# Performance work log

Measured on AMD Instinct MI355X. Metric: run time of the kernel, lower is better.

The kernel has to match this reference:

```python
import jax, jax.numpy as jnp
import numpy as np

N, E, IN_DIM, OUT_DIM, R = 50000, 800000, 128, 128, 8


def setup_inputs() -> dict:
    key = jax.random.key(0)
    k1, k2, k3, k4, k5 = jax.random.split(key, 5)
    x = jax.random.normal(k1, (N, IN_DIM), dtype=jnp.float32)
    edge_index = jax.random.randint(k2, (2, E), 0, N, dtype=jnp.int32)
    edge_type = jax.random.randint(k3, (E,), 0, R, dtype=jnp.int32)
    # Xavier-uniform-ish init for parameters
    lim_w = float(np.sqrt(6.0 / (IN_DIM + OUT_DIM)))
    weight = jax.random.uniform(k4, (R, IN_DIM, OUT_DIM), dtype=jnp.float32, minval=-lim_w, maxval=lim_w)
    self_weight = jax.random.uniform(k5, (IN_DIM, OUT_DIM), dtype=jnp.float32, minval=-lim_w, maxval=lim_w)
    return {"x": x, "weight": weight, "self_weight": self_weight,
            "edge_index": edge_index, "edge_type": edge_type}


def reference(x, weight, self_weight, edge_index, edge_type):
    n = x.shape[0]
    r = weight.shape[0]
    d_out = weight.shape[2]
    src, dst = edge_index[0], edge_index[1]
    # undirected: symmetrize edges (directed=False)
    src_all = jnp.concatenate([src, dst])          # [2E]
    dst_all = jnp.concatenate([dst, src])          # [2E]
    et_all = jnp.concatenate([edge_type, edge_type])  # [2E]
    # transform all nodes by every relation weight once: [R, N, D_out]
    xw = jnp.einsum('ni,rio->rno', x, weight)
    # gather per-edge messages already transformed by their relation's W_r
    msg = xw[et_all, src_all]                      # [2E, D_out]
    # fused (relation, dst) segment id -> per-relation scatter-add
    seg = et_all.astype(jnp.int32) * n + dst_all
    agg = jax.ops.segment_sum(msg, seg, num_segments=r * n).reshape(r, n, d_out)
    deg = jax.ops.segment_sum(jnp.ones_like(seg, dtype=x.dtype), seg,
                              num_segments=r * n).reshape(r, n)
    deg_inv = jnp.where(deg > 0, 1.0 / jnp.maximum(deg, 1.0), jnp.zeros_like(deg))
    out = jnp.sum(agg * deg_inv[..., None], axis=0)  # [N, D_out]
    out = out + x @ self_weight                       # self-loop
    return out
```

## Files before the change

### kernel.cpp

```cpp
#include <hip/hip_runtime.h>

#define NN 50000
#define EE 800000
#define RR 8
#define DD 128
#define SS (NN*RR)
#define TE (2*EE)
#define NB 782
#define NBLK 391
#define NS (NB*NBLK)

typedef __attribute__((ext_vector_type(8))) short bf16x8;
typedef __attribute__((ext_vector_type(4))) float f32x4;

__device__ __forceinline__ unsigned short f2bf(float f){
  unsigned int u = __float_as_uint(f);
  u += 0x7fffu + ((u >> 16) & 1u);
  return (unsigned short)(u >> 16);
}
__device__ __forceinline__ float bf_lo(unsigned int w){ return __uint_as_float(w << 16); }
__device__ __forceinline__ float bf_hi(unsigned int w){ return __uint_as_float(w & 0xffff0000u); }

__device__ __forceinline__ void acc8(float* a, uint4 u){
  a[0] += bf_lo(u.x); a[1] += bf_hi(u.x);
  a[2] += bf_lo(u.y); a[3] += bf_hi(u.y);
  a[4] += bf_lo(u.z); a[5] += bf_hi(u.z);
  a[6] += bf_lo(u.w); a[7] += bf_hi(u.w);
}
__device__ __forceinline__ unsigned int pack2(float a, float b){
  return ((unsigned int)f2bf(b) << 16) | (unsigned int)f2bf(a);
}

__device__ __forceinline__ void dir_edge(const int* ei, const int* et, int j,
                                         int& s, int& d, int& t){
  if (j < EE){ s = ei[j]; d = ei[EE + j]; t = et[j]; }
  else { int jj = j - EE; s = ei[EE + jj]; d = ei[jj]; t = et[jj]; }
}

__global__ __launch_bounds__(256) void k_hist(const int* __restrict__ ei,
                                              const int* __restrict__ et,
                                              int* __restrict__ hist){
  __shared__ int h[NB];
  int tid = threadIdx.x, bid = blockIdx.x;
  for (int i = tid; i < NB; i += 256) h[i] = 0;
  __syncthreads();
  int j0 = bid*4096;
  for (int k = tid; k < 4096; k += 256){
    int j = j0 + k;
    if (j < TE){
      int s, d, t; dir_edge(ei, et, j, s, d, t);
      atomicAdd(&h[d >> 6], 1);
    }
  }
  __syncthreads();
  for (int i = tid; i < NB; i += 256) hist[i*NBLK + bid] = h[i];
}

__global__ __launch_bounds__(256) void k_scan1(int* __restrict__ hist,
                                               int* __restrict__ blksum){
  __shared__ int sd[256];
  int b = blockIdx.x, tid = threadIdx.x;
  int base = b*1024 + tid*4;
  int v0 = (base+0 < NS) ? hist[base+0] : 0;
  int v1 = (base+1 < NS) ? hist[base+1] : 0;
  int v2 = (base+2 < NS) ? hist[base+2] : 0;
  int v3 = (base+3 < NS) ? hist[base+3] : 0;
  int ts = v0+v1+v2+v3;
  sd[tid] = ts; __syncthreads();
  for (int o = 1; o < 256; o <<= 1){
    int t = (tid >= o) ? sd[tid-o] : 0;
    __syncthreads();
    sd[tid] += t;
    __syncthreads();
  }
  int ex = sd[tid] - ts;
  if (base+0 < NS) hist[base+0] = ex; ex += v0;
  if (base+1 < NS) hist[base+1] = ex; ex += v1;
  if (base+2 < NS) hist[base+2] = ex; ex += v2;
  if (base+3 < NS) hist[base+3] = ex;
  if (tid == 255) blksum[b] = sd[255];
}

__global__ __launch_bounds__(512) void k_scan2(int* __restrict__ blksum, int nb){
  __shared__ int sd[512];
  int tid = threadIdx.x;
  int v = (tid < nb) ? blksum[tid] : 0;
  sd[tid] = v; __syncthreads();
  for (int o = 1; o < 512; o <<= 1){
    int t = (tid >= o) ? sd[tid-o] : 0;
    __syncthreads();
    sd[tid] += t;
    __syncthreads();
  }
  if (tid < nb) blksum[tid] = sd[tid] - v;
}

__global__ __launch_bounds__(256) void k_scan3(int* __restrict__ hist,
                                               const int* __restrict__ blksum){
  int i = blockIdx.x*blockDim.x + threadIdx.x;
  if (i < NS) hist[i] += blksum[i >> 10];
}

__global__ __launch_bounds__(256) void k_part(const int* __restrict__ ei,
                                              const int* __restrict__ et,
                                              const int* __restrict__ S,
                                              unsigned int* __restrict__ P){
  __shared__ int cur[NB];
  int tid = threadIdx.x, bid = blockIdx.x;
  for (int i = tid; i < NB; i += 256) cur[i] = S[i*NBLK + bid];
  __syncthreads();
  int j0 = bid*4096;
  for (int k = tid; k < 4096; k += 256){
    int j = j0 + k;
    if (j < TE){
      int s, d, t; dir_edge(ei, et, j, s, d, t);
      int b = d >> 6;
      int p = atomicAdd(&cur[b], 1);
      P[p] = (unsigned int)s | ((unsigned int)(d & 63) << 17)
           | ((unsigned int)t << 23);
    }
  }
}

__global__ __launch_bounds__(256) void k_build(const unsigned int* __restrict__ P,
                                               const int* __restrict__ S,
                                               int* __restrict__ esrc,
                                               int* __restrict__ offs){
  __shared__ int h[512], cu[512], sd[256];
  int tid = threadIdx.x, b = blockIdx.x;
  int pstart = S[b*NBLK];
  int pend   = (b+1 < NB) ? S[(b+1)*NBLK] : TE;
  int ne = pend - pstart;
  h[2*tid] = 0; h[2*tid+1] = 0;
  __syncthreads();
  for (int k = tid; k < ne; k += 256){
    unsigned int u = P[pstart + k];
    int lseg = (int)(((u >> 17) & 63u)*8u + (u >> 23));
    atomicAdd(&h[lseg], 1);
  }
  __syncthreads();
  int v0 = h[2*tid], v1 = h[2*tid+1];
  int ts = v0 + v1;
  sd[tid] = ts; __syncthreads();
  for (int o = 1; o < 256; o <<= 1){
    int t = (tid >= o) ? sd[tid-o] : 0;
    __syncthreads();
    sd[tid] += t;
    __syncthreads();
  }
  int ex = sd[tid] - ts;
  cu[2*tid]   = pstart + ex;
  cu[2*tid+1] = pstart + ex + v0;
  int seg0 = b*512;
  if (seg0 + 2*tid     < SS) offs[seg0 + 2*tid]     = cu[2*tid];
  if (seg0 + 2*tid + 1 < SS) offs[seg0 + 2*tid + 1] = cu[2*tid+1];
  if (b == NB-1 && tid == 0) offs[SS] = TE;
  __syncthreads();
  for (int k = tid; k < ne; k += 256){
    unsigned int u = P[pstart + k];
    int lseg = (int)(((u >> 17) & 63u)*8u + (u >> 23));
    int r = atomicAdd(&cu[lseg], 1);
    esrc[r] = (int)(u & 0x1ffffu);
  }
}

__global__ __launch_bounds__(256) void k_conv(const float* __restrict__ x,
                                              const float* __restrict__ w,
                                              const float* __restrict__ sw,
                                              unsigned short* __restrict__ xb,
                                              unsigned short* __restrict__ wb){
  int i = blockIdx.x*blockDim.x + threadIdx.x;
  const int M1 = NN*DD/4;
  if (i < M1){
    float4 v = ((const float4*)x)[i];
    ushort4 o;
    o.x = f2bf(v.x); o.y = f2bf(v.y); o.z = f2bf(v.z); o.w = f2bf(v.w);
    ((ushort4*)xb)[i] = o;
  } else {
    int j = i - M1;
    if (j < 9*DD*DD){
      int r = j >> 14; int rem = j & 16383; int n = rem >> 7; int k = rem & 127;
      float v = (r < 8) ? w[r*16384 + k*128 + n] : sw[k*128 + n];
      wb[j] = f2bf(v);
    }
  }
}

__global__ __launch_bounds__(256, 3) void k_fused(
    const unsigned short* __restrict__ xb,
    const unsigned short* __restrict__ wb,
    const int* __restrict__ offs,
    const int* __restrict__ esrc,
    float* __restrict__ out)
{
  __shared__ __align__(16) unsigned short Alds[2][32][136];
  const int tid  = threadIdx.x;
  const int wave = tid >> 6, lane = tid & 63;
  const int l15  = lane & 15, quad = lane >> 4;
  const int g    = quad;
  const int gl   = l15;
  const int lb   = g << 4;
  const int rowbase = blockIdx.x * 32;

  uint4 selfU[2];
  #pragma unroll
  for (int p = 0; p < 2; ++p){
    int gd = rowbase + wave*8 + 2*g + p;
    selfU[p] = make_uint4(0u,0u,0u,0u);
    if (gd < NN) selfU[p] = *(const uint4*)(xb + (size_t)gd*DD + gl*8);
  }

  int sidx = (rowbase + wave*8)*8 + lane;
  int voff = 0, vcnt = 0;
  if (sidx < SS){
    voff = offs[sidx];
    vcnt = offs[sidx + 1] - voff;
  }

  int idxbuf[2][2];
  uint4 U[2][8];

  auto issue_idx = [&](int rq, int bi){
    #pragma unroll
    for (int p = 0; p < 2; ++p){
      int sl  = (2*g + p)*8 + rq;
      int off = __shfl(voff, sl);
      int cnt = __shfl(vcnt, sl);
      idxbuf[bi][p] = 0;
      if (gl < cnt) idxbuf[bi][p] = esrc[off + gl];
    }
  };

  auto issue_bursts = [&](int rq, int bi){
    #pragma unroll
    for (int p = 0; p < 2; ++p){
      int sl  = (2*g + p)*8 + rq;
      int cnt = __shfl(vcnt, sl);
      int cm  = cnt < 8 ? cnt : 8;
      #pragma unroll
      for (int e = 0; e < 8; ++e){
        U[p][e] = make_uint4(0u,0u,0u,0u);
        if (e < cm){
          int s = __shfl(idxbuf[bi][p], lb + e);
          U[p][e] = *(const uint4*)(xb + (size_t)s*DD + gl*8);
        }
      }
    }
  };

  auto finish = [&](int rq, int bi, int lbuf){
    #pragma unroll
    for (int p = 0; p < 2; ++p){
      int sl  = (2*g + p)*8 + rq;
      int cnt = __shfl(vcnt, sl);
      int off = __shfl(voff, sl);
      float a[8] = {0.f,0.f,0.f,0.f,0.f,0.f,0.f,0.f};
      #pragma unroll
      for (int e = 0; e < 8; ++e) acc8(a, U[p][e]);
      int cm16 = cnt < 16 ? cnt : 16;
      for (int e2 = 8; e2 < cm16; ++e2){
        int s = __shfl(idxbuf[bi][p], lb + e2);
        uint4 u = *(const uint4*)(xb + (size_t)s*DD + gl*8);
        acc8(a, u);
      }
      for (int e2 = 16; e2 < cnt; ++e2){
        int s = esrc[off + e2];
        uint4 u = *(const uint4*)(xb + (size_t)s*DD + gl*8);
        acc8(a, u);
      }
      float sc = (cnt > 0) ? (1.0f / (float)cnt) : 0.f;
      uint4 w0;
      w0.x = pack2(a[0]*sc, a[1]*sc);
      w0.y = pack2(a[2]*sc, a[3]*sc);
      w0.z = pack2(a[4]*sc, a[5]*sc);
      w0.w = pack2(a[6]*sc, a[7]*sc);
      int rowl = wave*8 + 2*g + p;
      *(uint4*)&Alds[lbuf][rowl][gl*8] = w0;
    }
  };

  issue_idx(0, 0);
  issue_idx(1, 1);
  issue_bursts(0, 0);
  finish(0, 0, 0);
  __syncthreads();

  f32x4 C[2][2];
  #pragma unroll
  for (int m = 0; m < 2; ++m){ C[m][0] = (f32x4)(0.f); C[m][1] = (f32x4)(0.f); }

  #pragma unroll
  for (int rr = 0; rr < 9; ++rr){
    const unsigned short* wr = wb + rr * 16384;
    bf16x8 bfrag[2][4];
    #pragma unroll
    for (int nt = 0; nt < 2; ++nt)
      #pragma unroll
      for (int ks = 0; ks < 4; ++ks)
        bfrag[nt][ks] = *(const bf16x8*)(wr + (wave*32 + nt*16 + l15)*128 + ks*32 + quad*8);

    if (rr < 7) issue_bursts(rr + 1, (rr + 1) & 1);
    if (rr <= 5) issue_idx(rr + 2, rr & 1);

    #pragma unroll
    for (int m = 0; m < 2; ++m){
      #pragma unroll
      for (int ks = 0; ks < 4; ++ks){
        bf16x8 af = *(const bf16x8*)&Alds[rr & 1][m*16 + l15][ks*32 + quad*8];
        C[m][0] = __builtin_amdgcn_mfma_f32_16x16x32_bf16(af, bfrag[0][ks], C[m][0], 0, 0, 0);
        C[m][1] = __builtin_amdgcn_mfma_f32_16x16x32_bf16(af, bfrag[1][ks], C[m][1], 0, 0, 0);
      }
    }

    if (rr < 7) finish(rr + 1, (rr + 1) & 1, (rr + 1) & 1);
    if (rr == 7){
      #pragma unroll
      for (int p = 0; p < 2; ++p){
        int rowl = wave*8 + 2*g + p;
        *(uint4*)&Alds[0][rowl][gl*8] = selfU[p];
      }
    }
    if (rr < 8) __syncthreads();
  }

  #pragma unroll
  for (int m = 0; m < 2; ++m){
    #pragma unroll
    for (int nt = 0; nt < 2; ++nt){
      #pragma unroll
      for (int i = 0; i < 4; ++i){
        int row = m*16 + quad*4 + i;
        int gd  = rowbase + row;
        int col = wave*32 + nt*16 + l15;
        if (gd < NN) out[gd*DD + col] = C[m][nt][i];
      }
    }
  }
}

extern "C" void kernel_launch(void* const* d_in, const int* in_sizes, int n_in,
                              void* d_out, int out_size, void* d_ws, size_t ws_size,
                              hipStream_t stream){
  const float* x  = (const float*)d_in[0];
  const float* w  = (const float*)d_in[1];
  const float* sw = (const float*)d_in[2];
  const int*   ei = (const int*)d_in[3];
  const int*   et = (const int*)d_in[4];
  float* out = (float*)d_out;
  char* ws = (char*)d_ws;

  if (ws_size < (size_t)21100000) return;

  unsigned short* xb = (unsigned short*)(ws + 0);
  int*          hist = (int*)(ws + 0);
  int*        blksum = (int*)(ws + 1223168);
  unsigned int*    P = (unsigned int*)(ws + 1225216);
  int*          esrc = (int*)(ws + 12800000);
  int*          offs = (int*)(ws + 19200000);
  unsigned short* wb = (unsigned short*)(ws + 20800016);

  k_hist <<<NBLK, 256, 0, stream>>>(ei, et, hist);
  k_scan1<<<(NS + 1023)/1024, 256, 0, stream>>>(hist, blksum);
  k_scan2<<<1, 512, 0, stream>>>(blksum, (NS + 1023)/1024);
  k_scan3<<<(NS + 255)/256, 256, 0, stream>>>(hist, blksum);
  k_part <<<NBLK, 256, 0, stream>>>(ei, et, hist, P);
  k_build<<<NB, 256, 0, stream>>>(P, hist, esrc, offs);
  k_conv <<<(NN*DD/4 + 9*DD*DD + 255)/256, 256, 0, stream>>>(x, w, sw, xb, wb);
  k_fused<<<(NN + 31)/32, 256, 0, stream>>>(xb, wb, offs, esrc, out);
}
```

Baseline: 257.6 us.

## Precompute per-relation transformed features then gather-aggregate instead of aggregate-then-GEMM

Replaces the fused aggregate-then-multiply kernel with two kernels. The first is an MFMA GEMM that computes X·W_r for all 8 relations plus the self weight into a bf16 buffer. The second is a pure gather kernel that sums pre-transformed rows per destination, scaled by each relation's inverse degree. The relation id is packed into the esrc entries so a single pass over all of a node's edges works. This trades roughly 9x more GEMM output and a large ~115MB intermediate for a simpler, fully parallel gather; it falls back to the old kernel if the workspace is too small.

```diff
diff --git a/kernel.cpp b/kernel.cpp
--- a/kernel.cpp
+++ b/kernel.cpp
@@ -26,6 +26,12 @@
   a[2] += bf_lo(u.y); a[3] += bf_hi(u.y);
   a[4] += bf_lo(u.z); a[5] += bf_hi(u.z);
   a[6] += bf_lo(u.w); a[7] += bf_hi(u.w);
+}
+__device__ __forceinline__ void acc8s(float* a, uint4 u, float s){
+  a[0] += s*bf_lo(u.x); a[1] += s*bf_hi(u.x);
+  a[2] += s*bf_lo(u.y); a[3] += s*bf_hi(u.y);
+  a[4] += s*bf_lo(u.z); a[5] += s*bf_hi(u.z);
+  a[6] += s*bf_lo(u.w); a[7] += s*bf_hi(u.w);
 }
 __device__ __forceinline__ unsigned int pack2(float a, float b){
   return ((unsigned int)f2bf(b) << 16) | (unsigned int)f2bf(a);
@@ -160,7 +166,7 @@
     unsigned int u = P[pstart + k];
     int lseg = (int)(((u >> 17) & 63u)*8u + (u >> 23));
     int r = atomicAdd(&cu[lseg], 1);
-    esrc[r] = (int)(u & 0x1ffffu);
+    esrc[r] = (int)(u & 0x1ffffu) | (int)(((u >> 23) & 7u) << 17);
   }
 }
 
@@ -186,7 +192,107 @@
   }
 }
 
-__global__ __launch_bounds__(256, 3) void k_fused(
+
+__global__ __launch_bounds__(256, 2) void k_xw(
+    const unsigned short* __restrict__ xb,
+    const unsigned short* __restrict__ wb,
+    unsigned short* __restrict__ xw)
+{
+  const int tid  = threadIdx.x;
+  const int wave = tid >> 6, lane = tid & 63;
+  const int l15  = lane & 15, quad = lane >> 4;
+  const int row0 = blockIdx.x * 64 + wave * 16;
+
+  bf16x8 af[4];
+  {
+    int gr = row0 + l15; if (gr >= NN) gr = NN - 1;
+    #pragma unroll
+    for (int ks = 0; ks < 4; ++ks)
+      af[ks] = *(const bf16x8*)(xb + (size_t)gr*DD + ks*32 + quad*8);
+  }
+
+  #pragma unroll 1
+  for (int r = 0; r < 9; ++r){
+    const unsigned short* wr = wb + r * 16384;
+    bf16x8 bfrag[8][4];
+    #pragma unroll
+    for (int nt = 0; nt < 8; ++nt)
+      #pragma unroll
+      for (int ks = 0; ks < 4; ++ks)
+        bfrag[nt][ks] = *(const bf16x8*)(wr + (nt*16 + l15)*128 + ks*32 + quad*8);
+
+    f32x4 C[8];
+    #pragma unroll
+    for (int nt = 0; nt < 8; ++nt) C[nt] = (f32x4)(0.f);
+    #pragma unroll
+    for (int ks = 0; ks < 4; ++ks)
+      #pragma unroll
+      for (int nt = 0; nt < 8; ++nt)
+        C[nt] = __builtin_amdgcn_mfma_f32_16x16x32_bf16(af[ks], bfrag[nt][ks], C[nt], 0, 0, 0);
+
+    unsigned short* xs = xw + (size_t)r * NN * DD;
+    #pragma unroll
+    for (int nt = 0; nt < 8; ++nt)
+      #pragma unroll
+      for (int i = 0; i < 4; ++i){
+        int gr = row0 + quad*4 + i;
+        if (gr < NN) xs[(size_t)gr*DD + nt*16 + l15] = f2bf(C[nt][i]);
+      }
+  }
+}
+
+__global__ __launch_bounds__(256, 4) void k_agg(
+    const unsigned short* __restrict__ xw,
+    const int* __restrict__ offs,
+    const int* __restrict__ esrc,
+    float* __restrict__ out)
+{
+  const int tid   = threadIdx.x;
+  const int lane  = tid & 63;
+  const int gl    = lane & 15;
+  const int basel = lane & 48;
+  const int d     = blockIdx.x * 16 + (tid >> 4);
+
+  int o = 0;
+  if (gl < 9) o = offs[d*8 + gl];
+  int onx = __shfl(o, (basel + gl + 1) & 63);
+  int cnt = onx - o;
+  float scale = (gl < 8 && cnt > 0) ? 1.0f/(float)cnt : 0.0f;
+  int ebase = __shfl(o, basel);
+  int etot  = __shfl(o, basel + 8) - ebase;
+
+  float a[8] = {0.f,0.f,0.f,0.f,0.f,0.f,0.f,0.f};
+
+  for (int e = 0; e < etot; e += 12){
+    uint4 U[12]; float sc[12];
+    #pragma unroll
+    for (int s = 0; s < 12; ++s){
+      sc[s] = 0.f;
+      U[s] = make_uint4(0u,0u,0u,0u);
+      if (e + s < etot){
+        int pk  = esrc[ebase + e + s];
+        int rel = (pk >> 17) & 7;
+        sc[s]   = __shfl(scale, basel + rel);
+        int src = pk & 0x1ffff;
+        U[s] = *(const uint4*)(xw + ((size_t)rel*NN + src)*DD + gl*8);
+      }
+    }
+    #pragma unroll
+    for (int s = 0; s < 12; ++s) acc8s(a, U[s], sc[s]);
+  }
+
+  {
+    uint4 u = *(const uint4*)(xw + ((size_t)8*NN + d)*DD + gl*8);
+    acc8(a, u);
+  }
+
+  float4 v0; v0.x = a[0]; v0.y = a[1]; v0.z = a[2]; v0.w = a[3];
+  float4 v1; v1.x = a[4]; v1.y = a[5]; v1.z = a[6]; v1.w = a[7];
+  *(float4*)(out + (size_t)d*DD + gl*8)     = v0;
+  *(float4*)(out + (size_t)d*DD + gl*8 + 4) = v1;
+}
+
+__global__ __launch_bounds__(256, 3) void k_fused_fb(
     const unsigned short* __restrict__ xb,
     const unsigned short* __restrict__ wb,
     const int* __restrict__ offs,
@@ -241,7 +347,7 @@
       for (int e = 0; e < 8; ++e){
         U[p][e] = make_uint4(0u,0u,0u,0u);
         if (e < cm){
-          int s = __shfl(idxbuf[bi][p], lb + e);
+          int s = __shfl(idxbuf[bi][p], lb + e) & 0x1ffff;
           U[p][e] = *(const uint4*)(xb + (size_t)s*DD + gl*8);
         }
       }
@@ -259,12 +365,12 @@
       for (int e = 0; e < 8; ++e) acc8(a, U[p][e]);
       int cm16 = cnt < 16 ? cnt : 16;
       for (int e2 = 8; e2 < cm16; ++e2){
-        int s = __shfl(idxbuf[bi][p], lb + e2);
+        int s = __shfl(idxbuf[bi][p], lb + e2) & 0x1ffff;
         uint4 u = *(const uint4*)(xb + (size_t)s*DD + gl*8);
         acc8(a, u);
       }
       for (int e2 = 16; e2 < cnt; ++e2){
-        int s = esrc[off + e2];
+        int s = esrc[off + e2] & 0x1ffff;
         uint4 u = *(const uint4*)(xb + (size_t)s*DD + gl*8);
         acc8(a, u);
       }
@@ -358,6 +464,7 @@
   int*          esrc = (int*)(ws + 12800000);
   int*          offs = (int*)(ws + 19200000);
   unsigned short* wb = (unsigned short*)(ws + 20800016);
+  unsigned short* xw = (unsigned short*)(ws + 21095168);
 
   k_hist <<<NBLK, 256, 0, stream>>>(ei, et, hist);
   k_scan1<<<(NS + 1023)/1024, 256, 0, stream>>>(hist, blksum);
@@ -366,5 +473,11 @@
   k_part <<<NBLK, 256, 0, stream>>>(ei, et, hist, P);
   k_build<<<NB, 256, 0, stream>>>(P, hist, esrc, offs);
   k_conv <<<(NN*DD/4 + 9*DD*DD + 255)/256, 256, 0, stream>>>(x, w, sw, xb, wb);
-  k_fused<<<(NN + 31)/32, 256, 0, stream>>>(xb, wb, offs, esrc, out);
-}
+
+  if (ws_size >= (size_t)136295168){
+    k_xw <<<(NN + 63)/64, 256, 0, stream>>>(xb, wb, xw);
+    k_agg<<<NN/16, 256, 0, stream>>>(xw, offs, esrc, out);
+  } else {
+    k_fused_fb<<<(NN + 31)/32, 256, 0, stream>>>(xb, wb, offs, esrc, out);
+  }
+}
```

Result: slower. 359.3 us (+39.5%).
